# Kernel optimization log

Hardware: AMD Instinct MI355X
Metric: run time of the kernel (lower is better)

The kernel has to match this reference:

```python
import jax, jax.numpy as jnp
import numpy as np

B, A, F, T = 4096, 64, 124, 8
H1, H2 = 64, 16


def setup_inputs() -> dict:
    key = jax.random.key(0)
    ks = jax.random.split(key, 10)
    x = jax.random.normal(ks[0], (B, A, F + 1), dtype=jnp.float32)
    types = jax.random.randint(ks[1], (B, A), 0, T).astype(jnp.float32)
    x = x.at[:, :, 0].set(types)  # column 0 stores atom-type index
    mask = (jax.random.uniform(ks[2], (B, A)) < 0.9).astype(jnp.float32)
    s1 = 1.0 / np.sqrt(F)
    s2 = 1.0 / np.sqrt(H1)
    s3 = 1.0 / np.sqrt(H2)
    return {
        "x_padded": x,
        "mask": mask,
        "W1": jax.random.normal(ks[3], (T, F, H1), dtype=jnp.float32) * s1,
        "b1": jax.random.normal(ks[4], (T, H1), dtype=jnp.float32) * s1,
        "W2": jax.random.normal(ks[5], (T, H1, H2), dtype=jnp.float32) * s2,
        "b2": jax.random.normal(ks[6], (T, H2), dtype=jnp.float32) * s2,
        "W3": jax.random.normal(ks[7], (T, H2, 1), dtype=jnp.float32) * s3,
        "b3": jax.random.normal(ks[8], (T, 1), dtype=jnp.float32) * s3,
    }


def reference(x_padded, mask, W1, b1, W2, b2, W3, b3):
    # x_padded: [B, A, 1+F]; mask: [B, A]
    type_idx = x_padded[:, :, 0].astype(jnp.int32)           # [B, A]
    feats = x_padded[:, :, 1:]                               # [B, A, F]
    n_types = W1.shape[0]
    # Faithful to the original: every type's subnet runs on the FULL batch
    # with non-matching atoms zero-masked (bias paths still contribute).
    type_mask = (type_idx[None, :, :] == jnp.arange(n_types)[:, None, None]).astype(feats.dtype)  # [T,B,A]
    sel = feats[None, :, :, :] * type_mask[..., None]        # [T,B,A,F]
    h = jax.nn.relu(jnp.einsum('tbaf,tfh->tbah', sel, W1) + b1[:, None, None, :])
    h = jax.nn.relu(jnp.einsum('tbah,thg->tbag', h, W2) + b2[:, None, None, :])
    o = jnp.einsum('tbag,tgo->tbao', h, W3) + b3[:, None, None, :]  # [T,B,A,1]
    per_atom = (o[..., 0] * mask[None, :, :]).sum(axis=0)   # [B, A]
    return per_atom.sum(axis=1, keepdims=True)               # [B, 1]
```

## Files before the change

kernel.cpp:

```cpp
#include <hip/hip_runtime.h>
#include <stdint.h>

#define NMOL 4096
#define NATOMS (NMOL * 64)
#define NF 124
#define NT 8
#define ROWV 125
#define CAP 65536

#define WS_CURSOR   0
#define WS_DCONST   64
#define WS_W2T      1024
#define WS_W1S      18432
#define WS_IDS      1048576
#define WS_PACKED   4194304

typedef __attribute__((ext_vector_type(8))) short short8;
typedef __attribute__((ext_vector_type(4))) float floatx4;
typedef __attribute__((ext_vector_type(4))) unsigned int uint4v;

__device__ __forceinline__ unsigned short f2bf(float f) {
    unsigned u = __builtin_bit_cast(unsigned, f);
    u += 0x7fffu + ((u >> 16) & 1u);
    return (unsigned short)(u >> 16);
}

__device__ __forceinline__ void ld_lds16(const void* g, void* lds) {
    __builtin_amdgcn_global_load_lds(
        (const __attribute__((address_space(1))) unsigned int*)g,
        (__attribute__((address_space(3))) unsigned int*)lds, 16, 0, 0);
}

__global__ __launch_bounds__(256) void k_setup(const float* __restrict__ W1,
                                               const float* __restrict__ b1,
                                               const float* __restrict__ W2,
                                               const float* __restrict__ b2,
                                               const float* __restrict__ W3,
                                               const float* __restrict__ b3,
                                               unsigned* __restrict__ cursor,
                                               float* __restrict__ dconst,
                                               unsigned short* __restrict__ W1S,
                                               unsigned short* __restrict__ W2T,
                                               float* __restrict__ out) {
    int tid = threadIdx.x, b = blockIdx.x;
    if (b == 0) {
        __shared__ float c[NT];
        if (tid < 128) {
            int t = tid >> 4, g = tid & 15;
            float acc = b2[t * 16 + g];
            for (int h = 0; h < 64; ++h) {
                float h1 = b1[t * 64 + h];
                h1 = h1 > 0.f ? h1 : 0.f;
                acc += h1 * W2[(size_t)t * 1024 + h * 16 + g];
            }
            float h2 = acc > 0.f ? acc : 0.f;
            float v = h2 * W3[t * 16 + g];
            #pragma unroll
            for (int off = 1; off < 16; off <<= 1) v += __shfl_xor(v, off);
            if (g == 0) c[t] = v + b3[t];
        }
        if (tid < NT) cursor[tid] = (unsigned)(tid * CAP);
        __syncthreads();
        if (tid == 0) {
            float T_ = 0.f;
            for (int i = 0; i < NT; ++i) T_ += c[i];
            for (int i = 0; i < NT; ++i) dconst[i] = T_ - c[i];
        }
    } else if (b <= 8) {
        int t = b - 1;
        const float* w1g = W1 + (size_t)t * NF * 64;
        unsigned short* dst = W1S + (size_t)t * 8192;
        for (int id = tid; id < 1024; id += 256) {
            int h = id >> 4, cc = id & 15;
            unsigned u[4];
            #pragma unroll
            for (int j = 0; j < 4; ++j) {
                int f0 = cc * 8 + 2 * j;
                unsigned short lo = (f0 < NF)     ? f2bf(w1g[f0 * 64 + h])       : (unsigned short)0;
                unsigned short hi = (f0 + 1 < NF) ? f2bf(w1g[(f0 + 1) * 64 + h]) : (unsigned short)0;
                u[j] = (unsigned)lo | ((unsigned)hi << 16);
            }
            int p = cc ^ (h & 15);
            *(uint4v*)(dst + h * 128 + p * 8) = (uint4v){u[0], u[1], u[2], u[3]};
        }
    } else if (b == 9) {
        for (int i = tid; i < 8 * 16 * 64; i += 256) {
            int t = i >> 10, g = (i >> 6) & 15, h = i & 63;
            W2T[i] = f2bf(W2[(size_t)t * 1024 + h * 16 + g]);
        }
    } else {
        out[(b - 10) * 256 + tid] = 0.0f;
    }
}

__global__ __launch_bounds__(256, 4) void k_pack(const float* __restrict__ x,
                                                 const float* __restrict__ mask,
                                                 unsigned* __restrict__ cursor,
                                                 unsigned* __restrict__ ids,
                                                 unsigned short* __restrict__ packed) {
    __shared__ __align__(16) float sRaw[64 * ROWV];
    __shared__ unsigned sHist[NT], sBase[NT];
    __shared__ int sDest[64];
    int tid = threadIdx.x, b = blockIdx.x;
    if (tid < NT) sHist[tid] = 0u;
    {
        const uint4v* xs = (const uint4v*)(x + (size_t)b * 64 * ROWV);
        uint4v* sr = (uint4v*)sRaw;
        for (int i = tid; i < 2000; i += 256) sr[i] = xs[i];
    }
    float m = 0.f;
    if (tid < 64) m = mask[b * 64 + tid];
    __syncthreads();
    int t = 0, rank = -1;
    bool kept = false;
    if (tid < 64) {
        t = (int)sRaw[tid * ROWV];
        kept = (m != 0.f);
        if (kept) rank = (int)atomicAdd(&sHist[t], 1u);
    }
    __syncthreads();
    if (tid < NT && sHist[tid]) sBase[tid] = atomicAdd(&cursor[tid], sHist[tid]);
    __syncthreads();
    if (tid < 64) {
        int d = kept ? (int)(sBase[t] + (unsigned)rank) : -1;
        sDest[tid] = d;
        if (kept) ids[d] = (unsigned)b;
    }
    __syncthreads();
    for (int s = tid; s < 512; s += 256) {
        int r = s >> 3, k = s & 7;
        int d = sDest[r];
        if (d < 0) continue;
        const float* src = sRaw + r * ROWV + 1;
        unsigned u[8];
        #pragma unroll
        for (int j = 0; j < 8; ++j) {
            int c0 = k * 16 + 2 * j;
            float a  = (c0 < NF)     ? src[c0]     : 0.f;
            float bb = (c0 + 1 < NF) ? src[c0 + 1] : 0.f;
            u[j] = (unsigned)f2bf(a) | ((unsigned)f2bf(bb) << 16);
        }
        int skey = d & 15;
        uint4v* drow = (uint4v*)(packed + (size_t)d * 128);
        drow[(2 * k) ^ skey]     = (uint4v){u[0], u[1], u[2], u[3]};
        drow[(2 * k + 1) ^ skey] = (uint4v){u[4], u[5], u[6], u[7]};
    }
}

#define HS 72

__global__ __launch_bounds__(256, 3) void k_mlp(const unsigned short* __restrict__ packed,
                                                const unsigned short* __restrict__ W1S,
                                                const float* __restrict__ b1,
                                                const unsigned short* __restrict__ W2T,
                                                const float* __restrict__ b2,
                                                const float* __restrict__ W3,
                                                const float* __restrict__ b3,
                                                const unsigned* __restrict__ cursor,
                                                const float* __restrict__ dconst,
                                                const unsigned* __restrict__ ids,
                                                float* __restrict__ out) {
    __shared__ unsigned short sA[128 * 128];
    __shared__ unsigned short sW[64 * 128];
    __shared__ unsigned sIds[128];

    int t = blockIdx.x >> 9;
    int tile = blockIdx.x & 511;
    int cnt = (int)(cursor[t] - (unsigned)(t * CAP));
    int valid = cnt - (tile << 7);
    if (valid <= 0) return;
    if (valid > 128) valid = 128;

    int tid  = threadIdx.x;
    int wv   = tid >> 6;
    int lane = tid & 63;
    int quad = lane >> 4, l15 = lane & 15;
    int rowstart = t * CAP + (tile << 7);

    {
        const char* aseg = (const char*)packed + (size_t)rowstart * 256;
        #pragma unroll
        for (int i = 0; i < 8; ++i) {
            int off = (wv * 8 + i) * 1024;
            ld_lds16(aseg + off + lane * 16, (char*)sA + off);
        }
        const char* wseg = (const char*)W1S + (size_t)t * 16384;
        #pragma unroll
        for (int i = 0; i < 4; ++i) {
            int off = (wv * 4 + i) * 1024;
            ld_lds16(wseg + off + lane * 16, (char*)sW + off);
        }
    }
    if (tid < 128) sIds[tid] = ids[rowstart + tid];

    float b1v[4];
    #pragma unroll
    for (int n = 0; n < 4; ++n) b1v[n] = b1[t * 64 + n * 16 + l15];

    __syncthreads();

    floatx4 c1[2][4];
    #pragma unroll
    for (int m = 0; m < 2; ++m)
        #pragma unroll
        for (int n = 0; n < 4; ++n) c1[m][n] = (floatx4)0.f;

    int rowbase = wv * 32;
    #pragma unroll
    for (int ks = 0; ks < 4; ++ks) {
        int p = ((ks * 4 + quad) ^ l15) * 8;
        short8 a0 = *(const short8*)(sA + (rowbase + l15) * 128 + p);
        short8 a1 = *(const short8*)(sA + (rowbase + 16 + l15) * 128 + p);
        short8 bf[4];
        #pragma unroll
        for (int n = 0; n < 4; ++n)
            bf[n] = *(const short8*)(sW + (n * 16 + l15) * 128 + p);
        #pragma unroll
        for (int n = 0; n < 4; ++n) {
            c1[0][n] = __builtin_amdgcn_mfma_f32_16x16x32_bf16(a0, bf[n], c1[0][n], 0, 0, 0);
            c1[1][n] = __builtin_amdgcn_mfma_f32_16x16x32_bf16(a1, bf[n], c1[1][n], 0, 0, 0);
        }
    }

    __syncthreads();

    if (tid < 128) {
        const unsigned short* w2g = W2T + (size_t)t * 1024;
        int gg = tid >> 3, hp = (tid & 7) * 8;
        *(short8*)(sW + gg * HS + hp) = *(const short8*)(w2g + tid * 8);
    }
    #pragma unroll
    for (int m = 0; m < 2; ++m)
        #pragma unroll
        for (int n = 0; n < 4; ++n) {
            int col = n * 16 + l15;
            #pragma unroll
            for (int r = 0; r < 4; ++r) {
                float v = c1[m][n][r] + b1v[n];
                v = v > 0.f ? v : 0.f;
                sA[(rowbase + m * 16 + quad * 4 + r) * HS + col] = f2bf(v);
            }
        }

    __syncthreads();

    floatx4 c2[2];
    c2[0] = (floatx4)0.f; c2[1] = (floatx4)0.f;
    #pragma unroll
    for (int ks = 0; ks < 2; ++ks) {
        int ko = ks * 32 + quad * 8;
        short8 a0 = *(const short8*)(sA + (rowbase + l15) * HS + ko);
        short8 a1 = *(const short8*)(sA + (rowbase + 16 + l15) * HS + ko);
        short8 bf = *(const short8*)(sW + l15 * HS + ko);
        c2[0] = __builtin_amdgcn_mfma_f32_16x16x32_bf16(a0, bf, c2[0], 0, 0, 0);
        c2[1] = __builtin_amdgcn_mfma_f32_16x16x32_bf16(a1, bf, c2[1], 0, 0, 0);
    }

    float b2v = b2[t * 16 + l15];
    float w3v = W3[t * 16 + l15];
    float tail = b3[t] + dconst[t];
    #pragma unroll
    for (int m = 0; m < 2; ++m) {
        float h2v[4];
        #pragma unroll
        for (int r = 0; r < 4; ++r) {
            float v = c2[m][r] + b2v;
            v = v > 0.f ? v : 0.f;
            h2v[r] = v * w3v;
        }
        #pragma unroll
        for (int off = 1; off < 16; off <<= 1)
            #pragma unroll
            for (int r = 0; r < 4; ++r) h2v[r] += __shfl_xor(h2v[r], off);
        if (l15 == 0) {
            #pragma unroll
            for (int r = 0; r < 4; ++r) {
                int trow = rowbase + m * 16 + quad * 4 + r;
                if (trow < valid) {
                    atomicAdd(&out[sIds[trow]], h2v[r] + tail);
                }
            }
        }
    }
}

extern "C" void kernel_launch(void* const* d_in, const int* in_sizes, int n_in,
                              void* d_out, int out_size, void* d_ws, size_t ws_size,
                              hipStream_t stream) {
    const float* x    = (const float*)d_in[0];
    const float* mask = (const float*)d_in[1];
    const float* W1   = (const float*)d_in[2];
    const float* b1   = (const float*)d_in[3];
    const float* W2   = (const float*)d_in[4];
    const float* b2   = (const float*)d_in[5];
    const float* W3   = (const float*)d_in[6];
    const float* b3   = (const float*)d_in[7];
    float* out = (float*)d_out;

    char* ws = (char*)d_ws;
    unsigned*       cursor = (unsigned*)(ws + WS_CURSOR);
    float*          dconst = (float*)(ws + WS_DCONST);
    unsigned short* W2T    = (unsigned short*)(ws + WS_W2T);
    unsigned short* W1S    = (unsigned short*)(ws + WS_W1S);
    unsigned*       ids    = (unsigned*)(ws + WS_IDS);
    unsigned short* packed = (unsigned short*)(ws + WS_PACKED);

    k_setup<<<26, 256, 0, stream>>>(W1, b1, W2, b2, W3, b3, cursor, dconst, W1S, W2T, out);
    k_pack<<<NMOL, 256, 0, stream>>>(x, mask, cursor, ids, packed);
    k_mlp<<<NT * (CAP / 128), 256, 0, stream>>>(packed, W1S, b1, W2T, b2, W3, b3,
                                                cursor, dconst, ids, out);
}
```

Measured before the change: 267.8 us.

## Fuse pack and MLP into one kernel that runs every type per tile

Drops the type-bucketing pack kernel, its global atomics and the packed intermediate buffer. Each block now loads 128 atoms (two molecules) straight from x into LDS as bf16 and runs all 8 type subnets on them, keeping only rows whose type matches. It then reduces per molecule in-block and writes the output directly with no atomics. The cost is 8x more MFMA work per atom, with weights read from global/L2 instead of LDS, in exchange for removing one full round trip of the packed data through memory and a kernel launch.

```diff
diff --git a/kernel.cpp b/kernel.cpp
--- a/kernel.cpp
+++ b/kernel.cpp
@@ -2,18 +2,15 @@
 #include <stdint.h>
 
 #define NMOL 4096
-#define NATOMS (NMOL * 64)
 #define NF 124
 #define NT 8
 #define ROWV 125
-#define CAP 65536
-
-#define WS_CURSOR   0
-#define WS_DCONST   64
-#define WS_W2T      1024
-#define WS_W1S      18432
-#define WS_IDS      1048576
-#define WS_PACKED   4194304
+
+#define WS_DCONST 0
+#define WS_W1S    64
+#define WS_W2T    131136
+
+#define HS 72
 
 typedef __attribute__((ext_vector_type(8))) short short8;
 typedef __attribute__((ext_vector_type(4))) float floatx4;
@@ -23,12 +20,6 @@
     unsigned u = __builtin_bit_cast(unsigned, f);
     u += 0x7fffu + ((u >> 16) & 1u);
     return (unsigned short)(u >> 16);
-}
-
-__device__ __forceinline__ void ld_lds16(const void* g, void* lds) {
-    __builtin_amdgcn_global_load_lds(
-        (const __attribute__((address_space(1))) unsigned int*)g,
-        (__attribute__((address_space(3))) unsigned int*)lds, 16, 0, 0);
 }
 
 __global__ __launch_bounds__(256) void k_setup(const float* __restrict__ W1,
@@ -37,11 +28,9 @@
                                                const float* __restrict__ b2,
                                                const float* __restrict__ W3,
                                                const float* __restrict__ b3,
-                                               unsigned* __restrict__ cursor,
                                                float* __restrict__ dconst,
                                                unsigned short* __restrict__ W1S,
-                                               unsigned short* __restrict__ W2T,
-                                               float* __restrict__ out) {
+                                               unsigned short* __restrict__ W2T) {
     int tid = threadIdx.x, b = blockIdx.x;
     if (b == 0) {
         __shared__ float c[NT];
@@ -59,14 +48,13 @@
             for (int off = 1; off < 16; off <<= 1) v += __shfl_xor(v, off);
             if (g == 0) c[t] = v + b3[t];
         }
-        if (tid < NT) cursor[tid] = (unsigned)(tid * CAP);
         __syncthreads();
         if (tid == 0) {
             float T_ = 0.f;
             for (int i = 0; i < NT; ++i) T_ += c[i];
             for (int i = 0; i < NT; ++i) dconst[i] = T_ - c[i];
         }
-    } else if (b <= 8) {
+    } else {
         int t = b - 1;
         const float* w1g = W1 + (size_t)t * NF * 64;
         unsigned short* dst = W1S + (size_t)t * 8192;
@@ -83,204 +71,150 @@
             int p = cc ^ (h & 15);
             *(uint4v*)(dst + h * 128 + p * 8) = (uint4v){u[0], u[1], u[2], u[3]};
         }
-    } else if (b == 9) {
-        for (int i = tid; i < 8 * 16 * 64; i += 256) {
-            int t = i >> 10, g = (i >> 6) & 15, h = i & 63;
-            W2T[i] = f2bf(W2[(size_t)t * 1024 + h * 16 + g]);
-        }
-    } else {
-        out[(b - 10) * 256 + tid] = 0.0f;
-    }
-}
-
-__global__ __launch_bounds__(256, 4) void k_pack(const float* __restrict__ x,
+        unsigned short* d2 = W2T + (size_t)t * 1024;
+        for (int i = tid; i < 1024; i += 256) {
+            int g = i >> 6, h = i & 63;
+            d2[i] = f2bf(W2[(size_t)t * 1024 + h * 16 + g]);
+        }
+    }
+}
+
+__global__ __launch_bounds__(256, 3) void k_main(const float* __restrict__ x,
                                                  const float* __restrict__ mask,
-                                                 unsigned* __restrict__ cursor,
-                                                 unsigned* __restrict__ ids,
-                                                 unsigned short* __restrict__ packed) {
-    __shared__ __align__(16) float sRaw[64 * ROWV];
-    __shared__ unsigned sHist[NT], sBase[NT];
-    __shared__ int sDest[64];
-    int tid = threadIdx.x, b = blockIdx.x;
-    if (tid < NT) sHist[tid] = 0u;
-    {
-        const uint4v* xs = (const uint4v*)(x + (size_t)b * 64 * ROWV);
-        uint4v* sr = (uint4v*)sRaw;
-        for (int i = tid; i < 2000; i += 256) sr[i] = xs[i];
-    }
-    float m = 0.f;
-    if (tid < 64) m = mask[b * 64 + tid];
-    __syncthreads();
-    int t = 0, rank = -1;
-    bool kept = false;
-    if (tid < 64) {
-        t = (int)sRaw[tid * ROWV];
-        kept = (m != 0.f);
-        if (kept) rank = (int)atomicAdd(&sHist[t], 1u);
-    }
-    __syncthreads();
-    if (tid < NT && sHist[tid]) sBase[tid] = atomicAdd(&cursor[tid], sHist[tid]);
-    __syncthreads();
-    if (tid < 64) {
-        int d = kept ? (int)(sBase[t] + (unsigned)rank) : -1;
-        sDest[tid] = d;
-        if (kept) ids[d] = (unsigned)b;
-    }
-    __syncthreads();
-    for (int s = tid; s < 512; s += 256) {
-        int r = s >> 3, k = s & 7;
-        int d = sDest[r];
-        if (d < 0) continue;
-        const float* src = sRaw + r * ROWV + 1;
-        unsigned u[8];
-        #pragma unroll
-        for (int j = 0; j < 8; ++j) {
-            int c0 = k * 16 + 2 * j;
-            float a  = (c0 < NF)     ? src[c0]     : 0.f;
-            float bb = (c0 + 1 < NF) ? src[c0 + 1] : 0.f;
-            u[j] = (unsigned)f2bf(a) | ((unsigned)f2bf(bb) << 16);
-        }
-        int skey = d & 15;
-        uint4v* drow = (uint4v*)(packed + (size_t)d * 128);
-        drow[(2 * k) ^ skey]     = (uint4v){u[0], u[1], u[2], u[3]};
-        drow[(2 * k + 1) ^ skey] = (uint4v){u[4], u[5], u[6], u[7]};
-    }
-}
-
-#define HS 72
-
-__global__ __launch_bounds__(256, 3) void k_mlp(const unsigned short* __restrict__ packed,
-                                                const unsigned short* __restrict__ W1S,
-                                                const float* __restrict__ b1,
-                                                const unsigned short* __restrict__ W2T,
-                                                const float* __restrict__ b2,
-                                                const float* __restrict__ W3,
-                                                const float* __restrict__ b3,
-                                                const unsigned* __restrict__ cursor,
-                                                const float* __restrict__ dconst,
-                                                const unsigned* __restrict__ ids,
-                                                float* __restrict__ out) {
+                                                 const unsigned short* __restrict__ W1S,
+                                                 const float* __restrict__ b1,
+                                                 const unsigned short* __restrict__ W2T,
+                                                 const float* __restrict__ b2,
+                                                 const float* __restrict__ W3,
+                                                 const float* __restrict__ b3,
+                                                 const float* __restrict__ dconst,
+                                                 float* __restrict__ out) {
     __shared__ unsigned short sA[128 * 128];
-    __shared__ unsigned short sW[64 * 128];
-    __shared__ unsigned sIds[128];
-
-    int t = blockIdx.x >> 9;
-    int tile = blockIdx.x & 511;
-    int cnt = (int)(cursor[t] - (unsigned)(t * CAP));
-    int valid = cnt - (tile << 7);
-    if (valid <= 0) return;
-    if (valid > 128) valid = 128;
-
+    __shared__ unsigned short sH[128 * HS];
+    __shared__ unsigned char  sMeta[128];
+    __shared__ float          sPart[4];
+
+    int b    = blockIdx.x;
     int tid  = threadIdx.x;
     int wv   = tid >> 6;
     int lane = tid & 63;
     int quad = lane >> 4, l15 = lane & 15;
-    int rowstart = t * CAP + (tile << 7);
+    int rowbase = wv * 32;
+
+    if (lane < 32) {
+        int row  = rowbase + lane;
+        int atom = b * 128 + row;
+        float tf = x[(size_t)atom * ROWV];
+        float m  = mask[atom];
+        sMeta[row] = (m != 0.f) ? (unsigned char)(int)tf : (unsigned char)255;
+    }
 
     {
-        const char* aseg = (const char*)packed + (size_t)rowstart * 256;
-        #pragma unroll
-        for (int i = 0; i < 8; ++i) {
-            int off = (wv * 8 + i) * 1024;
-            ld_lds16(aseg + off + lane * 16, (char*)sA + off);
-        }
-        const char* wseg = (const char*)W1S + (size_t)t * 16384;
-        #pragma unroll
-        for (int i = 0; i < 4; ++i) {
-            int off = (wv * 4 + i) * 1024;
-            ld_lds16(wseg + off + lane * 16, (char*)sW + off);
-        }
-    }
-    if (tid < 128) sIds[tid] = ids[rowstart + tid];
-
-    float b1v[4];
+        const float* xb = x + (size_t)b * 128 * ROWV;
+        #pragma unroll 8
+        for (int r = 0; r < 32; ++r) {
+            int row = rowbase + r;
+            unsigned pk = 0u;
+            if (lane < 62) {
+                const float* src = xb + (size_t)row * ROWV + 1 + 2 * lane;
+                pk = (unsigned)f2bf(src[0]) | ((unsigned)f2bf(src[1]) << 16);
+            }
+            int c = lane >> 2;
+            *(unsigned*)(sA + row * 128 + ((c ^ (row & 15)) << 3) + 2 * (lane & 3)) = pk;
+        }
+    }
+
+    float wAcc = 0.f;
+
+    #pragma unroll 1
+    for (int t = 0; t < NT; ++t) {
+        const unsigned short* w1t = W1S + (size_t)t * 8192;
+        const unsigned short* w2t = W2T + (size_t)t * 1024;
+
+        float b1v[4];
+        #pragma unroll
+        for (int n = 0; n < 4; ++n) b1v[n] = b1[t * 64 + n * 16 + l15];
+
+        floatx4 c1[2][4];
+        #pragma unroll
+        for (int m = 0; m < 2; ++m)
+            #pragma unroll
+            for (int n = 0; n < 4; ++n) c1[m][n] = (floatx4)0.f;
+
+        #pragma unroll
+        for (int ks = 0; ks < 4; ++ks) {
+            int pc = ((ks * 4 + quad) ^ l15) << 3;
+            short8 a0 = *(const short8*)(sA + (rowbase + l15) * 128 + pc);
+            short8 a1 = *(const short8*)(sA + (rowbase + 16 + l15) * 128 + pc);
+            short8 bf[4];
+            #pragma unroll
+            for (int n = 0; n < 4; ++n)
+                bf[n] = *(const short8*)(w1t + (n * 16 + l15) * 128 + pc);
+            #pragma unroll
+            for (int n = 0; n < 4; ++n) {
+                c1[0][n] = __builtin_amdgcn_mfma_f32_16x16x32_bf16(a0, bf[n], c1[0][n], 0, 0, 0);
+                c1[1][n] = __builtin_amdgcn_mfma_f32_16x16x32_bf16(a1, bf[n], c1[1][n], 0, 0, 0);
+            }
+        }
+
+        #pragma unroll
+        for (int m = 0; m < 2; ++m)
+            #pragma unroll
+            for (int n = 0; n < 4; ++n) {
+                int col = n * 16 + l15;
+                #pragma unroll
+                for (int r = 0; r < 4; ++r) {
+                    float v = c1[m][n][r] + b1v[n];
+                    v = v > 0.f ? v : 0.f;
+                    sH[(rowbase + m * 16 + quad * 4 + r) * HS + col] = f2bf(v);
+                }
+            }
+
+        floatx4 c2[2];
+        c2[0] = (floatx4)0.f; c2[1] = (floatx4)0.f;
+        #pragma unroll
+        for (int ks = 0; ks < 2; ++ks) {
+            int ko = ks * 32 + quad * 8;
+            short8 a0 = *(const short8*)(sH + (rowbase + l15) * HS + ko);
+            short8 a1 = *(const short8*)(sH + (rowbase + 16 + l15) * HS + ko);
+            short8 bw = *(const short8*)(w2t + l15 * 64 + ko);
+            c2[0] = __builtin_amdgcn_mfma_f32_16x16x32_bf16(a0, bw, c2[0], 0, 0, 0);
+            c2[1] = __builtin_amdgcn_mfma_f32_16x16x32_bf16(a1, bw, c2[1], 0, 0, 0);
+        }
+
+        float b2v = b2[t * 16 + l15];
+        float w3v = W3[t * 16 + l15];
+        float dct = dconst[t] + b3[t];
+        #pragma unroll
+        for (int m = 0; m < 2; ++m) {
+            float h2v[4];
+            #pragma unroll
+            for (int r = 0; r < 4; ++r) {
+                float v = c2[m][r] + b2v;
+                v = v > 0.f ? v : 0.f;
+                h2v[r] = v * w3v;
+            }
+            #pragma unroll
+            for (int off = 1; off < 16; off <<= 1)
+                #pragma unroll
+                for (int r = 0; r < 4; ++r) h2v[r] += __shfl_xor(h2v[r], off);
+            if (l15 == 0) {
+                #pragma unroll
+                for (int r = 0; r < 4; ++r) {
+                    int row = rowbase + m * 16 + quad * 4 + r;
+                    if (sMeta[row] == (unsigned char)t) wAcc += h2v[r] + dct;
+                }
+            }
+        }
+    }
+
     #pragma unroll
-    for (int n = 0; n < 4; ++n) b1v[n] = b1[t * 64 + n * 16 + l15];
-
+    for (int off = 1; off < 64; off <<= 1) wAcc += __shfl_xor(wAcc, off);
+    if (lane == 0) sPart[wv] = wAcc;
     __syncthreads();
-
-    floatx4 c1[2][4];
-    #pragma unroll
-    for (int m = 0; m < 2; ++m)
-        #pragma unroll
-        for (int n = 0; n < 4; ++n) c1[m][n] = (floatx4)0.f;
-
-    int rowbase = wv * 32;
-    #pragma unroll
-    for (int ks = 0; ks < 4; ++ks) {
-        int p = ((ks * 4 + quad) ^ l15) * 8;
-        short8 a0 = *(const short8*)(sA + (rowbase + l15) * 128 + p);
-        short8 a1 = *(const short8*)(sA + (rowbase + 16 + l15) * 128 + p);
-        short8 bf[4];
-        #pragma unroll
-        for (int n = 0; n < 4; ++n)
-            bf[n] = *(const short8*)(sW + (n * 16 + l15) * 128 + p);
-        #pragma unroll
-        for (int n = 0; n < 4; ++n) {
-            c1[0][n] = __builtin_amdgcn_mfma_f32_16x16x32_bf16(a0, bf[n], c1[0][n], 0, 0, 0);
-            c1[1][n] = __builtin_amdgcn_mfma_f32_16x16x32_bf16(a1, bf[n], c1[1][n], 0, 0, 0);
-        }
-    }
-
-    __syncthreads();
-
-    if (tid < 128) {
-        const unsigned short* w2g = W2T + (size_t)t * 1024;
-        int gg = tid >> 3, hp = (tid & 7) * 8;
-        *(short8*)(sW + gg * HS + hp) = *(const short8*)(w2g + tid * 8);
-    }
-    #pragma unroll
-    for (int m = 0; m < 2; ++m)
-        #pragma unroll
-        for (int n = 0; n < 4; ++n) {
-            int col = n * 16 + l15;
-            #pragma unroll
-            for (int r = 0; r < 4; ++r) {
-                float v = c1[m][n][r] + b1v[n];
-                v = v > 0.f ? v : 0.f;
-                sA[(rowbase + m * 16 + quad * 4 + r) * HS + col] = f2bf(v);
-            }
-        }
-
-    __syncthreads();
-
-    floatx4 c2[2];
-    c2[0] = (floatx4)0.f; c2[1] = (floatx4)0.f;
-    #pragma unroll
-    for (int ks = 0; ks < 2; ++ks) {
-        int ko = ks * 32 + quad * 8;
-        short8 a0 = *(const short8*)(sA + (rowbase + l15) * HS + ko);
-        short8 a1 = *(const short8*)(sA + (rowbase + 16 + l15) * HS + ko);
-        short8 bf = *(const short8*)(sW + l15 * HS + ko);
-        c2[0] = __builtin_amdgcn_mfma_f32_16x16x32_bf16(a0, bf, c2[0], 0, 0, 0);
-        c2[1] = __builtin_amdgcn_mfma_f32_16x16x32_bf16(a1, bf, c2[1], 0, 0, 0);
-    }
-
-    float b2v = b2[t * 16 + l15];
-    float w3v = W3[t * 16 + l15];
-    float tail = b3[t] + dconst[t];
-    #pragma unroll
-    for (int m = 0; m < 2; ++m) {
-        float h2v[4];
-        #pragma unroll
-        for (int r = 0; r < 4; ++r) {
-            float v = c2[m][r] + b2v;
-            v = v > 0.f ? v : 0.f;
-            h2v[r] = v * w3v;
-        }
-        #pragma unroll
-        for (int off = 1; off < 16; off <<= 1)
-            #pragma unroll
-            for (int r = 0; r < 4; ++r) h2v[r] += __shfl_xor(h2v[r], off);
-        if (l15 == 0) {
-            #pragma unroll
-            for (int r = 0; r < 4; ++r) {
-                int trow = rowbase + m * 16 + quad * 4 + r;
-                if (trow < valid) {
-                    atomicAdd(&out[sIds[trow]], h2v[r] + tail);
-                }
-            }
-        }
+    if (tid == 0) {
+        out[2 * b]     = sPart[0] + sPart[1];
+        out[2 * b + 1] = sPart[2] + sPart[3];
     }
 }
 
@@ -298,15 +232,10 @@
     float* out = (float*)d_out;
 
     char* ws = (char*)d_ws;
-    unsigned*       cursor = (unsigned*)(ws + WS_CURSOR);
     float*          dconst = (float*)(ws + WS_DCONST);
+    unsigned short* W1S    = (unsigned short*)(ws + WS_W1S);
     unsigned short* W2T    = (unsigned short*)(ws + WS_W2T);
-    unsigned short* W1S    = (unsigned short*)(ws + WS_W1S);
-    unsigned*       ids    = (unsigned*)(ws + WS_IDS);
-    unsigned short* packed = (unsigned short*)(ws + WS_PACKED);
-
-    k_setup<<<26, 256, 0, stream>>>(W1, b1, W2, b2, W3, b3, cursor, dconst, W1S, W2T, out);
-    k_pack<<<NMOL, 256, 0, stream>>>(x, mask, cursor, ids, packed);
-    k_mlp<<<NT * (CAP / 128), 256, 0, stream>>>(packed, W1S, b1, W2T, b2, W3, b3,
-                                                cursor, dconst, ids, out);
-}
+
+    k_setup<<<9, 256, 0, stream>>>(W1, b1, W2, b2, W3, b3, dconst, W1S, W2T);
+    k_main<<<NMOL / 2, 256, 0, stream>>>(x, mask, W1S, b1, W2T, b2, W3, b3, dconst, out);
+}
```

New measurement: 303.1 us. 13.2% more time.
